# Kernel tuning notes

Hardware: AMD Instinct MI355X
Metric: run time of the kernel (lower is better)

The kernel has to match this reference:

```python
import jax, jax.numpy as jnp
import numpy as np
from jax import lax

B, C, H, W = 32, 1, 512, 512

def kernel_gauss_2d(m=3, sigma=3):
    x = np.arange(-m, m + 0.1)
    X, Y = np.meshgrid(x, x)
    g = np.exp(-(X ** 2 + Y ** 2) / (2 * sigma ** 2))
    g /= np.sum(g)
    return g.astype(np.float32)

KERNEL33 = (0.25 * np.array([[0., 1., 0.], [1., 0., 1.], [0., 1., 0.]], dtype=np.float32))
KERNEL_GAUSS = kernel_gauss_2d(m=3, sigma=3)  # 7x7


def _conv(x, w, pad):
    # NCHW conv, stride 1, symmetric padding
    return lax.conv_general_dilated(
        x, w, window_strides=(1, 1), padding=[(pad, pad), (pad, pad)],
        dimension_numbers=("NCHW", "OIHW", "NCHW"))


def _maxpool(x, k, pad):
    return lax.reduce_window(
        x, -jnp.inf, lax.max,
        window_dimensions=(1, 1, k, k), window_strides=(1, 1, 1, 1),
        padding=[(0, 0), (0, 0), (pad, pad), (pad, pad)])


def setup_inputs() -> dict:
    key = jax.random.key(0)
    ks = jax.random.split(key, 9)
    d = {"X": jax.random.normal(ks[0], (B, C, H, W), dtype=jnp.float32)}
    d["w0"] = jax.random.normal(ks[1], (2, 1, 1, 1), dtype=jnp.float32) * 0.5
    d["b0"] = jax.random.normal(ks[2], (2,), dtype=jnp.float32) * 0.1
    for i in range(1, 7):
        d[f"w{i}"] = jax.random.normal(ks[2 + i], (2, 1, 1, 1), dtype=jnp.float32) * 0.5
    return d


def reference(X, w0, b0, w1, w2, w3, w4, w5, w6):
    k33 = jnp.asarray(KERNEL33).reshape(1, 1, 3, 3)
    kg = jnp.asarray(KERNEL_GAUSS).reshape(1, 1, 7, 7)

    X1 = _conv(X, k33, pad=1)                 # fixed 3x3 blur
    X2 = _conv(X, kg, pad=3)                  # fixed 7x7 gaussian
    X3 = -_maxpool(-X, 3, pad=1)              # 3x3 min-pool
    X4 = -_maxpool(-X, 11, pad=5)             # 11x11 min-pool
    X5 = _maxpool(X, 3, pad=1)                # 3x3 max-pool
    X6 = _maxpool(X, 11, pad=5)               # 11x11 max-pool

    out = _conv(X, w0, 0) + b0.reshape(1, 2, 1, 1)
    out = out + _conv(X1, w1, 0) + _conv(X2, w2, 0) + _conv(X3, w3, 0)
    out = out + _conv(X4, w4, 0) + _conv(X5, w5, 0) + _conv(X6, w6, 0)
    return out
```

## Files before the change

kernel.cpp:

```cpp
#include <hip/hip_runtime.h>

#define IMG 512
#define TW 64
#define TH 32
#define GROWS 38
#define PROWS 42
#define GST 64

typedef __fp16 h2v __attribute__((ext_vector_type(2)));
union UH { unsigned u; h2v h; };

__device__ __forceinline__ float nan0(float v){ return v==v ? v : 0.0f; }
__device__ __forceinline__ float min3f(float a,float b,float c){ return fminf(fminf(a,b),c); }
__device__ __forceinline__ float max3f(float a,float b,float c){ return fmaxf(fmaxf(a,b),c); }

__global__ __launch_bounds__(512)
void simplenet_fused(const float* __restrict__ X,
                     const float* __restrict__ w0, const float* __restrict__ b0,
                     const float* __restrict__ w1, const float* __restrict__ w2,
                     const float* __restrict__ w3, const float* __restrict__ w4,
                     const float* __restrict__ w5, const float* __restrict__ w6,
                     float* __restrict__ out)
{
    __shared__ float    GH [GROWS*GST];
    __shared__ unsigned HNX[PROWS*GST];

    const int tid = threadIdx.x;
    const int xo = tid & 63, ty = tid >> 6, y0 = ty*4;
    const int bx = blockIdx.x, by = blockIdx.y, bz = blockIdx.z;
    const int tx0 = bx*TW, ty0 = by*TH;
    const bool xe = (bx==0)||(bx==IMG/TW-1);
    const bool ye = (by==0)||(by==IMG/TH-1);
    const float* Xb = X + (size_t)bz*(IMG*IMG);
    const float qn = __builtin_nanf("");

    const float W0c0=w0[0], W0c1=w0[1], B0=b0[0], B1=b0[1];
    const float W1c0=w1[0], W1c1=w1[1], W2c0=w2[0], W2c1=w2[1];
    const float W3c0=w3[0], W3c1=w3[1], W4c0=w4[0], W4c1=w4[1];
    const float W5c0=w5[0], W5c1=w5[1], W6c0=w6[0], W6c1=w6[1];

    const float G0=0.10628875f, G1=0.14032194f, G2=0.16577342f, G3=0.17523179f;

    for (int t = tid; t < PROWS*16; t += 512) {
        const int r = t >> 4, g = t & 15;
        const int gy  = ty0 - 5 + r;
        const int gx0 = tx0 - 8 + 4*g;
        const int wb  = r*GST + 4*g;
        if ((unsigned)gy >= IMG) {
            *(uint4*)&HNX[wb] = make_uint4(0x7BFF7BFFu,0x7BFF7BFFu,0x7BFF7BFFu,0x7BFF7BFFu);
            if (r >= 2 && r < 40)
                *(float4*)&GH[(r-2)*GST+4*g] = make_float4(qn,qn,qn,qn);
            continue;
        }
        float x[20];
        const bool xs = (unsigned)gx0 > (unsigned)(IMG-20);
        if (!xs) {
#pragma unroll
            for (int j=0;j<5;++j) {
                const float4 q = *(const float4*)(Xb + gy*IMG + gx0 + 4*j);
                x[4*j]=q.x; x[4*j+1]=q.y; x[4*j+2]=q.z; x[4*j+3]=q.w;
            }
        } else {
            const float* row = Xb + gy*IMG;
#pragma unroll
            for (int i=0;i<20;++i) {
                const int gx = gx0 + i;
                const float v = row[min(max(gx,0),IMG-1)];
                x[i] = ((unsigned)gx < IMG) ? v : qn;
            }
        }
        float mn[12], mx[12];
#pragma unroll
        for (int i=0;i<12;++i) {
            mn[i] = min3f(x[i+3],x[i+4],x[i+5]);
            mx[i] = max3f(x[i+3],x[i+4],x[i+5]);
        }
        unsigned hw[4];
#pragma unroll
        for (int k=0;k<4;++k) {
            const float hn = fminf(fminf(mn[k],mn[k+3]), fminf(mn[k+6],mn[k+8]));
            const float hx = fmaxf(fmaxf(mx[k],mx[k+3]), fmaxf(mx[k+6],mx[k+8]));
            UH c; c.h = __builtin_amdgcn_cvt_pkrtz(hn, -hx);
            hw[k] = c.u;
        }
        *(uint4*)&HNX[wb] = make_uint4(hw[0],hw[1],hw[2],hw[3]);
        if (r >= 2 && r < 40) {
            float zz[10];
#pragma unroll
            for (int j=0;j<10;++j) zz[j] = xs ? nan0(x[5+j]) : x[5+j];
            float gh4[4];
#pragma unroll
            for (int k=0;k<4;++k)
                gh4[k] = G0*(zz[k]+zz[k+6]) + G1*(zz[k+1]+zz[k+5]) + G2*(zz[k+2]+zz[k+4]) + G3*zz[k+3];
            *(float4*)&GH[(r-2)*GST+4*g] = make_float4(gh4[0],gh4[1],gh4[2],gh4[3]);
        }
    }

    float a0[4], a1[4];

    {
        const int gxc = tx0 + xo;
        float L[6], C[6], R[6];
        if (!xe && !ye) {
#pragma unroll
            for (int i=0;i<6;++i) {
                const float* row = Xb + (ty0+y0-1+i)*IMG + gxc;
                L[i]=row[-1]; C[i]=row[0]; R[i]=row[1];
            }
        } else {
#pragma unroll
            for (int i=0;i<6;++i) {
                const int gy = ty0+y0-1+i;
                const bool yv = (unsigned)gy < IMG;
                const float* row = Xb + (yv ? gy : 0)*IMG;
                float l = row[max(gxc-1,0)], c = row[gxc], r = row[min(gxc+1,IMG-1)];
                if (!yv) { l=qn; c=qn; r=qn; }
                if (gxc==0)     l=qn;
                if (gxc==IMG-1) r=qn;
                L[i]=l; C[i]=c; R[i]=r;
            }
        }
        float hm[6], hx6[6];
#pragma unroll
        for (int i=0;i<6;++i) { hm[i]=min3f(L[i],C[i],R[i]); hx6[i]=max3f(L[i],C[i],R[i]); }
        float Lz[6], Rz[6];
#pragma unroll
        for (int i=0;i<6;++i) { Lz[i] = xe ? nan0(L[i]) : L[i];
                                Rz[i] = xe ? nan0(R[i]) : R[i]; }
        const float Cz0 = ye ? nan0(C[0]) : C[0];
        const float Cz5 = ye ? nan0(C[5]) : C[5];
        const float up[4]={Cz0,C[1],C[2],C[3]};
        const float dn[4]={C[2],C[3],C[4],Cz5};
#pragma unroll
        for (int p=0;p<4;++p) {
            const float cr = 0.25f*(up[p] + dn[p] + Lz[p+1] + Rz[p+1]);
            a0[p] = B0 + W0c0*C[p+1] + W1c0*cr;
            a1[p] = B1 + W0c1*C[p+1] + W1c1*cr;
            const float mnv = min3f(hm[p],hm[p+1],hm[p+2]);
            const float mxv = max3f(hx6[p],hx6[p+1],hx6[p+2]);
            a0[p] += W3c0*mnv + W5c0*mxv;
            a1[p] += W3c1*mnv + W5c1*mxv;
        }
    }
    __syncthreads();

    {
        float wv[10];
        h2v q[14];
#pragma unroll
        for (int i=0;i<10;++i) wv[i] = GH[(y0+i)*GST+xo];
#pragma unroll
        for (int i=0;i<14;++i) { UH uu; uu.u = HNX[(y0+i)*GST+xo]; q[i] = uu.h; }
        if (ye) {
#pragma unroll
            for (int i=0;i<10;++i) wv[i] = nan0(wv[i]);
        }
#pragma unroll
        for (int p=0;p<4;++p) {
            const float s = G0*(wv[p]+wv[p+6]) + G1*(wv[p+1]+wv[p+5])
                          + G2*(wv[p+2]+wv[p+4]) + G3*wv[p+3];
            a0[p] += W2c0*s; a1[p] += W2c1*s;
        }
        h2v s = q[10];
#pragma unroll
        for (int i=9;i>=4;--i) s = __builtin_elementwise_min(s, q[i]);
        const h2v S3 = __builtin_elementwise_min(s,  q[3]);
        const h2v S2 = __builtin_elementwise_min(S3, q[2]);
        const h2v S1 = __builtin_elementwise_min(S2, q[1]);
        const h2v S0 = __builtin_elementwise_min(S1, q[0]);
        const h2v p1 = q[11];
        const h2v p2 = __builtin_elementwise_min(p1, q[12]);
        const h2v p3 = __builtin_elementwise_min(p2, q[13]);
        const h2v o0 = S0;
        const h2v o1 = __builtin_elementwise_min(S1, p1);
        const h2v o2 = __builtin_elementwise_min(S2, p2);
        const h2v o3 = __builtin_elementwise_min(S3, p3);
        const float on[4] = {(float)o0[0], (float)o1[0], (float)o2[0], (float)o3[0]};
        const float ox[4] = {-(float)o0[1], -(float)o1[1], -(float)o2[1], -(float)o3[1]};
#pragma unroll
        for (int p=0;p<4;++p) {
            a0[p] += W4c0*on[p] + W6c0*ox[p];
            a1[p] += W4c1*on[p] + W6c1*ox[p];
        }
    }

    float* o0p = out + ((size_t)bz*2 + 0)*(IMG*IMG) + (size_t)(ty0+y0)*IMG + tx0 + xo;
    float* o1p = o0p + (IMG*IMG);
#pragma unroll
    for (int p=0;p<4;++p) {
        o0p[(size_t)p*IMG] = a0[p];
        o1p[(size_t)p*IMG] = a1[p];
    }
}

extern "C" void kernel_launch(void* const* d_in, const int* in_sizes, int n_in,
                              void* d_out, int out_size, void* d_ws, size_t ws_size,
                              hipStream_t stream) {
    const float* X  = (const float*)d_in[0];
    const float* w0 = (const float*)d_in[1];
    const float* b0 = (const float*)d_in[2];
    const float* w1 = (const float*)d_in[3];
    const float* w2 = (const float*)d_in[4];
    const float* w3 = (const float*)d_in[5];
    const float* w4 = (const float*)d_in[6];
    const float* w5 = (const float*)d_in[7];
    const float* w6 = (const float*)d_in[8];
    float* out = (float*)d_out;

    dim3 grid(IMG/TW, IMG/TH, 32);
    simplenet_fused<<<grid, 512, 0, stream>>>(X, w0, b0, w1, w2, w3, w4, w5, w6, out);
}
```

Baseline: 39.08 us.

## Rebalance halo preprocessing across all threads and zero-fill out-of-image rows

The halo preprocessing loop (42 rows x 16 groups = 672 work items) previously ran in two passes over 512 threads, so the second pass left most threads idle. Now threads 0-351 handle rows 0-21 with 4-column groups and threads 352-511 handle rows 22-41 with 8-column groups, so every thread does one pass. Out-of-image Gaussian rows are written as zeros instead of NaN, which removes the later NaN-to-zero fixup on edge tiles. Launch bounds also request 8 blocks, which may cap register use; the wider groups raise register pressure and make per-thread work uneven.

```diff
diff --git a/kernel.cpp b/kernel.cpp
--- a/kernel.cpp
+++ b/kernel.cpp
@@ -14,7 +14,7 @@
 __device__ __forceinline__ float min3f(float a,float b,float c){ return fminf(fminf(a,b),c); }
 __device__ __forceinline__ float max3f(float a,float b,float c){ return fmaxf(fmaxf(a,b),c); }
 
-__global__ __launch_bounds__(512)
+__global__ __launch_bounds__(512, 8)
 void simplenet_fused(const float* __restrict__ X,
                      const float* __restrict__ w0, const float* __restrict__ b0,
                      const float* __restrict__ w1, const float* __restrict__ w2,
@@ -41,58 +41,117 @@
 
     const float G0=0.10628875f, G1=0.14032194f, G2=0.16577342f, G3=0.17523179f;
 
-    for (int t = tid; t < PROWS*16; t += 512) {
-        const int r = t >> 4, g = t & 15;
+    if (tid < 352) {
+        const int r = tid >> 4, g = tid & 15;
         const int gy  = ty0 - 5 + r;
         const int gx0 = tx0 - 8 + 4*g;
         const int wb  = r*GST + 4*g;
         if ((unsigned)gy >= IMG) {
             *(uint4*)&HNX[wb] = make_uint4(0x7BFF7BFFu,0x7BFF7BFFu,0x7BFF7BFFu,0x7BFF7BFFu);
-            if (r >= 2 && r < 40)
-                *(float4*)&GH[(r-2)*GST+4*g] = make_float4(qn,qn,qn,qn);
-            continue;
-        }
-        float x[20];
-        const bool xs = (unsigned)gx0 > (unsigned)(IMG-20);
-        if (!xs) {
-#pragma unroll
-            for (int j=0;j<5;++j) {
-                const float4 q = *(const float4*)(Xb + gy*IMG + gx0 + 4*j);
-                x[4*j]=q.x; x[4*j+1]=q.y; x[4*j+2]=q.z; x[4*j+3]=q.w;
-            }
+            if (r >= 2)
+                *(float4*)&GH[(r-2)*GST+4*g] = make_float4(0.f,0.f,0.f,0.f);
         } else {
-            const float* row = Xb + gy*IMG;
-#pragma unroll
-            for (int i=0;i<20;++i) {
-                const int gx = gx0 + i;
-                const float v = row[min(max(gx,0),IMG-1)];
-                x[i] = ((unsigned)gx < IMG) ? v : qn;
-            }
-        }
-        float mn[12], mx[12];
-#pragma unroll
-        for (int i=0;i<12;++i) {
-            mn[i] = min3f(x[i+3],x[i+4],x[i+5]);
-            mx[i] = max3f(x[i+3],x[i+4],x[i+5]);
-        }
-        unsigned hw[4];
-#pragma unroll
-        for (int k=0;k<4;++k) {
-            const float hn = fminf(fminf(mn[k],mn[k+3]), fminf(mn[k+6],mn[k+8]));
-            const float hx = fmaxf(fmaxf(mx[k],mx[k+3]), fmaxf(mx[k+6],mx[k+8]));
-            UH c; c.h = __builtin_amdgcn_cvt_pkrtz(hn, -hx);
-            hw[k] = c.u;
-        }
-        *(uint4*)&HNX[wb] = make_uint4(hw[0],hw[1],hw[2],hw[3]);
-        if (r >= 2 && r < 40) {
-            float zz[10];
-#pragma unroll
-            for (int j=0;j<10;++j) zz[j] = xs ? nan0(x[5+j]) : x[5+j];
-            float gh4[4];
-#pragma unroll
-            for (int k=0;k<4;++k)
-                gh4[k] = G0*(zz[k]+zz[k+6]) + G1*(zz[k+1]+zz[k+5]) + G2*(zz[k+2]+zz[k+4]) + G3*zz[k+3];
-            *(float4*)&GH[(r-2)*GST+4*g] = make_float4(gh4[0],gh4[1],gh4[2],gh4[3]);
+            float x[20];
+            const bool xs = (unsigned)gx0 > (unsigned)(IMG-20);
+            if (!xs) {
+#pragma unroll
+                for (int j=0;j<5;++j) {
+                    const float4 q = *(const float4*)(Xb + gy*IMG + gx0 + 4*j);
+                    x[4*j]=q.x; x[4*j+1]=q.y; x[4*j+2]=q.z; x[4*j+3]=q.w;
+                }
+            } else {
+                const float* row = Xb + gy*IMG;
+#pragma unroll
+                for (int i=0;i<20;++i) {
+                    const int gx = gx0 + i;
+                    const float v = row[min(max(gx,0),IMG-1)];
+                    x[i] = ((unsigned)gx < IMG) ? v : qn;
+                }
+            }
+            float mn[12], mx[12];
+#pragma unroll
+            for (int i=0;i<12;++i) {
+                mn[i] = min3f(x[i+3],x[i+4],x[i+5]);
+                mx[i] = max3f(x[i+3],x[i+4],x[i+5]);
+            }
+            unsigned hw[4];
+#pragma unroll
+            for (int k=0;k<4;++k) {
+                const float hn = fminf(fminf(mn[k],mn[k+3]), fminf(mn[k+6],mn[k+8]));
+                const float hx = fmaxf(fmaxf(mx[k],mx[k+3]), fmaxf(mx[k+6],mx[k+8]));
+                UH c; c.h = __builtin_amdgcn_cvt_pkrtz(hn, -hx);
+                hw[k] = c.u;
+            }
+            *(uint4*)&HNX[wb] = make_uint4(hw[0],hw[1],hw[2],hw[3]);
+            if (r >= 2) {
+                float zz[10];
+#pragma unroll
+                for (int j=0;j<10;++j) zz[j] = xs ? nan0(x[5+j]) : x[5+j];
+                float gh4[4];
+#pragma unroll
+                for (int k=0;k<4;++k)
+                    gh4[k] = G0*(zz[k]+zz[k+6]) + G1*(zz[k+1]+zz[k+5]) + G2*(zz[k+2]+zz[k+4]) + G3*zz[k+3];
+                *(float4*)&GH[(r-2)*GST+4*g] = make_float4(gh4[0],gh4[1],gh4[2],gh4[3]);
+            }
+        }
+    } else {
+        const int t = tid - 352;
+        const int r = 22 + (t >> 3), g = t & 7;
+        const int gy  = ty0 - 5 + r;
+        const int gx0 = tx0 - 8 + 8*g;
+        const int wb  = r*GST + 8*g;
+        if ((unsigned)gy >= IMG) {
+            *(uint4*)&HNX[wb]   = make_uint4(0x7BFF7BFFu,0x7BFF7BFFu,0x7BFF7BFFu,0x7BFF7BFFu);
+            *(uint4*)&HNX[wb+4] = make_uint4(0x7BFF7BFFu,0x7BFF7BFFu,0x7BFF7BFFu,0x7BFF7BFFu);
+            if (r < 40) {
+                *(float4*)&GH[(r-2)*GST+8*g]   = make_float4(0.f,0.f,0.f,0.f);
+                *(float4*)&GH[(r-2)*GST+8*g+4] = make_float4(0.f,0.f,0.f,0.f);
+            }
+        } else {
+            float x[24];
+            const bool xs = (unsigned)gx0 > (unsigned)(IMG-24);
+            if (!xs) {
+#pragma unroll
+                for (int j=0;j<6;++j) {
+                    const float4 q = *(const float4*)(Xb + gy*IMG + gx0 + 4*j);
+                    x[4*j]=q.x; x[4*j+1]=q.y; x[4*j+2]=q.z; x[4*j+3]=q.w;
+                }
+            } else {
+                const float* row = Xb + gy*IMG;
+#pragma unroll
+                for (int i=0;i<24;++i) {
+                    const int gx = gx0 + i;
+                    const float v = row[min(max(gx,0),IMG-1)];
+                    x[i] = ((unsigned)gx < IMG) ? v : qn;
+                }
+            }
+            float mn[16], mx[16];
+#pragma unroll
+            for (int i=0;i<16;++i) {
+                mn[i] = min3f(x[i+3],x[i+4],x[i+5]);
+                mx[i] = max3f(x[i+3],x[i+4],x[i+5]);
+            }
+            unsigned hw[8];
+#pragma unroll
+            for (int k=0;k<8;++k) {
+                const float hn = fminf(fminf(mn[k],mn[k+3]), fminf(mn[k+6],mn[k+8]));
+                const float hx = fmaxf(fmaxf(mx[k],mx[k+3]), fmaxf(mx[k+6],mx[k+8]));
+                UH c; c.h = __builtin_amdgcn_cvt_pkrtz(hn, -hx);
+                hw[k] = c.u;
+            }
+            *(uint4*)&HNX[wb]   = make_uint4(hw[0],hw[1],hw[2],hw[3]);
+            *(uint4*)&HNX[wb+4] = make_uint4(hw[4],hw[5],hw[6],hw[7]);
+            if (r < 40) {
+                float zz[14];
+#pragma unroll
+                for (int j=0;j<14;++j) zz[j] = xs ? nan0(x[5+j]) : x[5+j];
+                float gh8[8];
+#pragma unroll
+                for (int k=0;k<8;++k)
+                    gh8[k] = G0*(zz[k]+zz[k+6]) + G1*(zz[k+1]+zz[k+5]) + G2*(zz[k+2]+zz[k+4]) + G3*zz[k+3];
+                *(float4*)&GH[(r-2)*GST+8*g]   = make_float4(gh8[0],gh8[1],gh8[2],gh8[3]);
+                *(float4*)&GH[(r-2)*GST+8*g+4] = make_float4(gh8[4],gh8[5],gh8[6],gh8[7]);
+            }
         }
     }
 
@@ -151,10 +210,6 @@
         for (int i=0;i<10;++i) wv[i] = GH[(y0+i)*GST+xo];
 #pragma unroll
         for (int i=0;i<14;++i) { UH uu; uu.u = HNX[(y0+i)*GST+xo]; q[i] = uu.h; }
-        if (ye) {
-#pragma unroll
-            for (int i=0;i<10;++i) wv[i] = nan0(wv[i]);
-        }
 #pragma unroll
         for (int p=0;p<4;++p) {
             const float s = G0*(wv[p]+wv[p+6]) + G1*(wv[p+1]+wv[p+5])
```

Measured after the change: 37.47 us. 4.1% less time.
